# Optimization experiments

Measured on AMD Instinct MI355X. Metric: run time of the kernel, lower is better.

The kernel has to match this reference:

```python
import jax, jax.numpy as jnp
import numpy as np

N = 20000      # nodes
E = 256000     # edges
ESM = 1280     # esm_dim
H = 4          # heads
C = 256        # hidden_dim (per-head out)
HC = H * C     # 1024, concat width


def setup_inputs() -> dict:
    key = jax.random.key(0)
    ks = jax.random.split(key, 12)
    s = 0.02
    x = jax.random.normal(ks[0], (N, ESM), jnp.float32)
    edge_index = jax.random.randint(ks[1], (2, E), 0, N, dtype=jnp.int32)
    edge_weights = jax.random.uniform(ks[2], (E,), jnp.float32)
    # GATv2Conv params (PyG): lin_l (src, bias), lin_r (dst, no bias), lin_edge (no bias), att, out bias
    Wl = jax.random.normal(ks[3], (ESM, HC), jnp.float32) * s
    bl = jnp.zeros((HC,), jnp.float32)
    Wr = jax.random.normal(ks[4], (ESM, HC), jnp.float32) * s
    We = jax.random.normal(ks[5], (1, HC), jnp.float32) * s
    att = jax.random.normal(ks[6], (H, C), jnp.float32) * s
    b_gat = jnp.zeros((HC,), jnp.float32)
    # SAGEConv params: lin_l on mean-aggregated neighbors (bias), lin_r on root (no bias)
    Wsl = jax.random.normal(ks[7], (HC, ESM), jnp.float32) * s
    bsl = jnp.zeros((ESM,), jnp.float32)
    Wsr = jax.random.normal(ks[8], (HC, ESM), jnp.float32) * s
    # LayerNorm
    gamma = jnp.ones((ESM,), jnp.float32)
    beta = jnp.zeros((ESM,), jnp.float32)
    return dict(x=x, edge_index=edge_index, edge_weights=edge_weights,
                Wl=Wl, bl=bl, Wr=Wr, We=We, att=att, b_gat=b_gat,
                Wsl=Wsl, bsl=bsl, Wsr=Wsr, gamma=gamma, beta=beta)


def reference(x, edge_index, edge_weights, Wl, bl, Wr, We, att, b_gat,
              Wsl, bsl, Wsr, gamma, beta):
    src, dst = edge_index[0], edge_index[1]
    ew = edge_weights[:, None]                                    # [E,1]
    ones = jnp.ones((E,), x.dtype)
    deg = jax.ops.segment_sum(ones, dst, num_segments=N)          # in-degree [N]
    # ---- GATv2: add self-loops, edge_attr fill_value='mean' (mean of incoming attrs)
    loop_attr = jax.ops.segment_sum(ew, dst, num_segments=N) / jnp.maximum(deg, 1.0)[:, None]
    loop = jnp.arange(N, dtype=src.dtype)
    src_f = jnp.concatenate([src, loop])
    dst_f = jnp.concatenate([dst, loop])
    ea = jnp.concatenate([ew, loop_attr], axis=0)                 # [E+N,1]
    xl = (x @ Wl + bl).reshape(N, H, C)                           # source transform
    xr = (x @ Wr).reshape(N, H, C)                                # target transform
    ee = (ea @ We).reshape(-1, H, C)                              # edge transform
    m = jax.nn.leaky_relu(xl[src_f] + xr[dst_f] + ee, 0.2)        # [E+N,H,C]
    logits = jnp.einsum('ehc,hc->eh', m, att)                     # [E+N,H]
    amax = jax.ops.segment_max(logits, dst_f, num_segments=N)
    ex = jnp.exp(logits - amax[dst_f])
    den = jax.ops.segment_sum(ex, dst_f, num_segments=N)
    alpha = ex / (den[dst_f] + 1e-16)                             # softmax per dst node
    gat = jax.ops.segment_sum(alpha[:, :, None] * xl[src_f], dst_f, num_segments=N)
    gat = gat.reshape(N, HC) + b_gat
    h = jax.nn.elu(gat)
    # ---- SAGEConv: mean neighbor aggregation (no self loops) + root weight
    agg = jax.ops.segment_sum(h[src], dst, num_segments=N) / jnp.maximum(deg, 1.0)[:, None]
    y = jax.nn.relu(agg @ Wsl + bsl + h @ Wsr)
    # ---- residual + LayerNorm
    z = y + x
    mu = jnp.mean(z, axis=-1, keepdims=True)
    var = jnp.mean(jnp.square(z - mu), axis=-1, keepdims=True)
    return (z - mu) * jax.lax.rsqrt(var + 1e-5) * gamma + beta
```

## Files before the change

kernel.cpp:

```cpp
#include <hip/hip_runtime.h>
#include <hip/hip_bf16.h>
#include <math.h>

constexpr int kN   = 20000;
constexpr int kE   = 256000;
constexpr int kESM = 1280;
constexpr int kHC  = 1024;

typedef unsigned int  u32;
typedef unsigned short ushort_t;
typedef __bf16 bf16x8 __attribute__((ext_vector_type(8)));
typedef float  f32x4  __attribute__((ext_vector_type(4)));
typedef unsigned short u16x8 __attribute__((ext_vector_type(8)));
typedef unsigned short u16x4 __attribute__((ext_vector_type(4)));
typedef __attribute__((address_space(1))) const u32 gu32;
typedef __attribute__((address_space(3))) u32 lu32;

static __device__ __forceinline__ unsigned short f2bf_rne(float f) {
    u32 u = __float_as_uint(f);
    u32 r = (u + 0x7FFFu + ((u >> 16) & 1u)) >> 16;
    return (unsigned short)r;
}
static __device__ __forceinline__ float bf2f(unsigned short h) {
    return __uint_as_float(((u32)h) << 16);
}

__global__ __launch_bounds__(256) void deg_kernel(
    const int* __restrict__ dst, const float* __restrict__ ew,
    int* __restrict__ deg, float* __restrict__ wsum)
{
    int e = blockIdx.x * 256 + threadIdx.x;
    if (e < kE) {
        int d = dst[e];
        atomicAdd(&deg[d], 1);
        atomicAdd(&wsum[d], ew[e]);
    }
}

__global__ __launch_bounds__(256) void scan_kernel(
    const int* __restrict__ deg, float* __restrict__ loopat,
    int* __restrict__ offsets)
{
    __shared__ int s[256];
    int tid = threadIdx.x;
    int base = 0;
    if (tid == 0) offsets[0] = 0;
    for (int t0 = 0; t0 < kN; t0 += 256) {
        int i = t0 + tid;
        int d = (i < kN) ? deg[i] : 0;
        if (i < kN) {
            float w = loopat[i];
            loopat[i] = w / fmaxf((float)d, 1.0f);
        }
        s[tid] = d;
        int v = d;
        for (int off = 1; off < 256; off <<= 1) {
            __syncthreads();
            int add = (tid >= off) ? s[tid - off] : 0;
            __syncthreads();
            v += add;
            s[tid] = v;
        }
        __syncthreads();
        if (i < kN) offsets[i + 1] = base + v;
        base += s[255];
        __syncthreads();
    }
}

__global__ __launch_bounds__(256) void sort_kernel(
    const int* __restrict__ src, const int* __restrict__ dst,
    const float* __restrict__ ew, const int* __restrict__ offsets,
    int* __restrict__ cnt, int* __restrict__ ssrc, float* __restrict__ sew)
{
    int e = blockIdx.x * 256 + threadIdx.x;
    if (e < kE) {
        int d = dst[e];
        int p = offsets[d] + atomicAdd(&cnt[d], 1);
        ssrc[p] = src[e];
        sew[p]  = ew[e];
    }
}


__global__ __launch_bounds__(512) void pack_a_kernel(
    const float* __restrict__ A, int M, int K,
    int NKB, ushort_t* __restrict__ dst)
{
    const int kb = blockIdx.x, mb = blockIdx.y;
    const int tid = threadIdx.x;
    const int g = tid >> 7, r = tid & 127;
    const int row = mb * 128 + r;

    u16x8 hi, lo;
    if (row < M) {
        const float* src = A + (size_t)row * K + kb * 32 + g * 8;
        float4 v0 = *(const float4*)src;
        float4 v1 = *(const float4*)(src + 4);
        float vals[8] = {v0.x, v0.y, v0.z, v0.w, v1.x, v1.y, v1.z, v1.w};
#pragma unroll
        for (int j = 0; j < 8; ++j) {
            unsigned short h = f2bf_rne(vals[j]);
            hi[j] = h;
            lo[j] = f2bf_rne(vals[j] - bf2f(h));
        }
    } else {
#pragma unroll
        for (int j = 0; j < 8; ++j) { hi[j] = 0; lo[j] = 0; }
    }
    ushort_t* tb = dst + ((size_t)mb * NKB + kb) * 8192;
    *(u16x8*)&tb[0    + g * 1024 + r * 8] = hi;
    *(u16x8*)&tb[4096 + g * 1024 + r * 8] = lo;
}

__global__ __launch_bounds__(512) void pack_a2_kernel(
    const float* __restrict__ agg, const ushort_t* __restrict__ hb,
    int M, ushort_t* __restrict__ dst)
{
    const int kb = blockIdx.x, mb = blockIdx.y;
    const int tid = threadIdx.x;
    const int g = tid >> 7, r = tid & 127;
    const int row = mb * 128 + r;

    u16x8 hi, lo;
    if (row < M) {
        if (kb < 32) {
            const float* src = agg + (size_t)row * 1024 + kb * 32 + g * 8;
            float4 v0 = *(const float4*)src;
            float4 v1 = *(const float4*)(src + 4);
            float vals[8] = {v0.x, v0.y, v0.z, v0.w, v1.x, v1.y, v1.z, v1.w};
#pragma unroll
            for (int j = 0; j < 8; ++j) {
                unsigned short h = f2bf_rne(vals[j]);
                hi[j] = h;
                lo[j] = f2bf_rne(vals[j] - bf2f(h));
            }
        } else {
            hi = *(const u16x8*)&hb[(size_t)row * 1024 + (kb - 32) * 32 + g * 8];
#pragma unroll
            for (int j = 0; j < 8; ++j) lo[j] = 0;
        }
    } else {
#pragma unroll
        for (int j = 0; j < 8; ++j) { hi[j] = 0; lo[j] = 0; }
    }
    ushort_t* tb = dst + ((size_t)mb * 64 + kb) * 8192;
    *(u16x8*)&tb[0    + g * 1024 + r * 8] = hi;
    *(u16x8*)&tb[4096 + g * 1024 + r * 8] = lo;
}

__global__ __launch_bounds__(512) void pack_b_kernel(
    const float* __restrict__ B1, const float* __restrict__ B2,
    int N, int split, int mode, ushort_t* __restrict__ dst)
{
    const int kb = blockIdx.x, nb = blockIdx.y;
    const int NKB = gridDim.x;
    const int tid = threadIdx.x;
    const int g = tid >> 7, c = tid & 127;
    const int n = nb * 128 + c;

    u16x8 hi, lo;
#pragma unroll
    for (int j = 0; j < 8; ++j) {
        int k = kb * 32 + g * 8 + j;
        float v;
        if (mode == 0) {
            v = (n < split) ? B1[(size_t)k * split + n]
                            : B2[(size_t)k * (N - split) + (n - split)];
        } else {
            v = (k < split) ? B1[(size_t)k * N + n]
                            : B2[(size_t)(k - split) * N + n];
        }
        unsigned short h = f2bf_rne(v);
        hi[j] = h;
        lo[j] = f2bf_rne(v - bf2f(h));
    }
    ushort_t* tb = dst + ((size_t)nb * NKB + kb) * 8192;
    *(u16x8*)&tb[0    + g * 1024 + c * 8] = hi;
    *(u16x8*)&tb[4096 + g * 1024 + c * 8] = lo;
}

__global__ __launch_bounds__(256) void gemm_mfma(
    const ushort_t* __restrict__ Ap, const ushort_t* __restrict__ Bp,
    const float* __restrict__ bias, int biasN,
    const float* __restrict__ resid, float* __restrict__ C,
    int M, int N, int NKB, int do_relu)
{
    __shared__ ushort_t sb[16384];
    const int tid  = threadIdx.x;
    const int wid  = tid >> 6;
    const int lane = tid & 63;
    const int l15 = lane & 15, l4 = lane >> 4;
    const int mb = blockIdx.y, nb = blockIdx.x;
    const int wr = wid >> 1, wc = wid & 1;

    f32x4 acc[4][4];
#pragma unroll
    for (int i = 0; i < 4; ++i)
#pragma unroll
        for (int j = 0; j < 4; ++j) acc[i][j] = (f32x4){0.f, 0.f, 0.f, 0.f};

    const char* at = (const char*)(Ap + (size_t)mb * NKB * 8192);
    const char* bt = (const char*)(Bp + (size_t)nb * NKB * 8192);

    for (int kb = 0; kb < NKB; ++kb) {
        const char* atk = at + (size_t)kb * 16384;
        const char* btk = bt + (size_t)kb * 16384;
#pragma unroll
        for (int c = 0; c < 4; ++c) {
            __builtin_amdgcn_global_load_lds(
                (gu32*)(atk + c * 4096 + tid * 16),
                (lu32*)&sb[c * 2048 + wid * 512], 16, 0, 0);
            __builtin_amdgcn_global_load_lds(
                (gu32*)(btk + c * 4096 + tid * 16),
                (lu32*)&sb[8192 + c * 2048 + wid * 512], 16, 0, 0);
        }
        __syncthreads();

        bf16x8 af[2][4], bv[2][4];
#pragma unroll
        for (int hl = 0; hl < 2; ++hl)
#pragma unroll
            for (int m = 0; m < 4; ++m)
                af[hl][m] = *(const bf16x8*)&sb[hl * 4096 + l4 * 1024 + (wr * 64 + m * 16 + l15) * 8];
#pragma unroll
        for (int hl = 0; hl < 2; ++hl)
#pragma unroll
            for (int n = 0; n < 4; ++n)
                bv[hl][n] = *(const bf16x8*)&sb[8192 + hl * 4096 + l4 * 1024 + (wc * 64 + n * 16 + l15) * 8];

#pragma unroll
        for (int m = 0; m < 4; ++m)
#pragma unroll
            for (int n = 0; n < 4; ++n) {
                acc[m][n] = __builtin_amdgcn_mfma_f32_16x16x32_bf16(af[0][m], bv[0][n], acc[m][n], 0, 0, 0);
                acc[m][n] = __builtin_amdgcn_mfma_f32_16x16x32_bf16(af[0][m], bv[1][n], acc[m][n], 0, 0, 0);
                acc[m][n] = __builtin_amdgcn_mfma_f32_16x16x32_bf16(af[1][m], bv[0][n], acc[m][n], 0, 0, 0);
            }
        __syncthreads();
    }

    const int row_w = mb * 128 + wr * 64;
    const int col_w = nb * 128 + wc * 64;
#pragma unroll
    for (int m = 0; m < 4; ++m) {
#pragma unroll
        for (int n = 0; n < 4; ++n) {
            const int col = col_w + n * 16 + l15;
#pragma unroll
            for (int j = 0; j < 4; ++j) {
                const int row = row_w + m * 16 + l4 * 4 + j;
                if (row < M) {
                    float v = acc[m][n][j];
                    if (bias && col < biasN) v += bias[col];
                    if (do_relu) v = fmaxf(v, 0.f);
                    if (resid) v += resid[(size_t)row * N + col];
                    C[(size_t)row * N + col] = v;
                }
            }
        }
    }
}

__global__ __launch_bounds__(256) void gat2_kernel(
    const float* __restrict__ xlr, const int* __restrict__ ssrc,
    const float* __restrict__ sew, const int* __restrict__ offsets,
    const float* __restrict__ loopat, const float* __restrict__ We,
    const float* __restrict__ att, const float* __restrict__ bgat,
    ushort_t* __restrict__ hout)
{
    const int n = blockIdx.x;
    const int base = threadIdx.x * 4;

    const float4 xr4 = *(const float4*)&xlr[(size_t)n * 2048 + 1024 + base];
    const float4 We4 = *(const float4*)&We[base];
    const float4 at4 = *(const float4*)&att[base];

    float M = -INFINITY, D = 0.f;
    float4 acc = make_float4(0.f, 0.f, 0.f, 0.f);

    const int beg = offsets[n], end = offsets[n + 1];
    for (int e = beg; e <= end; ++e) {
        int s; float w;
        if (e < end) { s = ssrc[e]; w = sew[e]; }
        else         { s = n;       w = loopat[n]; }

        const float4 xls = *(const float4*)&xlr[(size_t)s * 2048 + base];
        float m0 = xls.x + xr4.x + w * We4.x;
        float m1 = xls.y + xr4.y + w * We4.y;
        float m2 = xls.z + xr4.z + w * We4.z;
        float m3 = xls.w + xr4.w + w * We4.w;
        m0 = (m0 >= 0.f) ? m0 : 0.2f * m0;
        m1 = (m1 >= 0.f) ? m1 : 0.2f * m1;
        m2 = (m2 >= 0.f) ? m2 : 0.2f * m2;
        m3 = (m3 >= 0.f) ? m3 : 0.2f * m3;
        float p = m0 * at4.x + m1 * at4.y + m2 * at4.z + m3 * at4.w;
#pragma unroll
        for (int o = 32; o >= 1; o >>= 1) p += __shfl_xor(p, o, 64);

        float newM  = fmaxf(M, p);
        float scale = __expf(M - newM);
        float wexp  = __expf(p - newM);
        D     = D * scale + wexp;
        acc.x = acc.x * scale + wexp * xls.x;
        acc.y = acc.y * scale + wexp * xls.y;
        acc.z = acc.z * scale + wexp * xls.z;
        acc.w = acc.w * scale + wexp * xls.w;
        M = newM;
    }

    const float inv = 1.0f / (D + 1e-16f);
    float g0 = acc.x * inv + bgat[base + 0];
    float g1 = acc.y * inv + bgat[base + 1];
    float g2 = acc.z * inv + bgat[base + 2];
    float g3 = acc.w * inv + bgat[base + 3];
    u16x4 hv;
    hv[0] = f2bf_rne((g0 > 0.f) ? g0 : expm1f(g0));
    hv[1] = f2bf_rne((g1 > 0.f) ? g1 : expm1f(g1));
    hv[2] = f2bf_rne((g2 > 0.f) ? g2 : expm1f(g2));
    hv[3] = f2bf_rne((g3 > 0.f) ? g3 : expm1f(g3));
    *(u16x4*)&hout[(size_t)n * 1024 + base] = hv;
}

__global__ __launch_bounds__(256) void agg2_kernel(
    const ushort_t* __restrict__ hb, const int* __restrict__ ssrc,
    const int* __restrict__ offsets, float* __restrict__ aggout)
{
    const int n = blockIdx.x;
    const int base = threadIdx.x * 4;
    float4 a = make_float4(0.f, 0.f, 0.f, 0.f);
    const int beg = offsets[n], end = offsets[n + 1];
    for (int e = beg; e < end; ++e) {
        const u16x4 hv = *(const u16x4*)&hb[(size_t)ssrc[e] * 1024 + base];
        a.x += bf2f(hv[0]); a.y += bf2f(hv[1]);
        a.z += bf2f(hv[2]); a.w += bf2f(hv[3]);
    }
    const float inv = 1.0f / fmaxf((float)(end - beg), 1.0f);
    a.x *= inv; a.y *= inv; a.z *= inv; a.w *= inv;
    *(float4*)&aggout[(size_t)n * 1024 + base] = a;
}

__global__ __launch_bounds__(320) void ln_kernel(
    float* __restrict__ z, const float* __restrict__ gamma,
    const float* __restrict__ beta)
{
    const int r = blockIdx.x;
    const int t = threadIdx.x;
    const int wave = t >> 6, lane = t & 63;
    __shared__ float red[5];

    float4 v = *(const float4*)&z[(size_t)r * kESM + t * 4];
    float s = v.x + v.y + v.z + v.w;
#pragma unroll
    for (int o = 32; o >= 1; o >>= 1) s += __shfl_xor(s, o, 64);
    if (lane == 0) red[wave] = s;
    __syncthreads();
    s = red[0] + red[1] + red[2] + red[3] + red[4];
    const float mu = s * (1.0f / (float)kESM);

    float dx = v.x - mu, dy = v.y - mu, dz = v.z - mu, dw = v.w - mu;
    float q = dx * dx + dy * dy + dz * dz + dw * dw;
#pragma unroll
    for (int o = 32; o >= 1; o >>= 1) q += __shfl_xor(q, o, 64);
    __syncthreads();
    if (lane == 0) red[wave] = q;
    __syncthreads();
    q = red[0] + red[1] + red[2] + red[3] + red[4];
    const float rstd = rsqrtf(q * (1.0f / (float)kESM) + 1e-5f);

    const float4 g4 = *(const float4*)&gamma[t * 4];
    const float4 b4 = *(const float4*)&beta[t * 4];
    float4 o;
    o.x = dx * rstd * g4.x + b4.x;
    o.y = dy * rstd * g4.y + b4.y;
    o.z = dz * rstd * g4.z + b4.z;
    o.w = dw * rstd * g4.w + b4.w;
    *(float4*)&z[(size_t)r * kESM + t * 4] = o;
}

#define BM 128
#define BN 128
#define BK 16

__global__ __launch_bounds__(256) void gemm_kernel(
    const float* __restrict__ A,  const float* __restrict__ B,
    const float* __restrict__ A2, const float* __restrict__ B2,
    const float* __restrict__ bias, const float* __restrict__ resid,
    float* __restrict__ C, int M, int N, int K, int do_relu)
{
    __shared__ float As[BK][BM];
    __shared__ float Bs[BK][BN];

    const int tid = threadIdx.x;
    const int bm = blockIdx.y, bn = blockIdx.x;
    const int row0 = bm * BM, col0 = bn * BN;
    const int tx = tid & 15, ty = tid >> 4;

    float acc[8][8];
#pragma unroll
    for (int i = 0; i < 8; ++i)
#pragma unroll
        for (int j = 0; j < 8; ++j) acc[i][j] = 0.0f;

    const int arow  = tid >> 1;
    const int akoff = (tid & 1) * 8;
    const int bkr   = tid >> 4;
    const int bcol  = (tid & 15) * 8;

    for (int pair = 0; pair < 2; ++pair) {
        const float* Ap = pair ? A2 : A;
        const float* Bp = pair ? B2 : B;
        if (!Ap) break;
        for (int k0 = 0; k0 < K; k0 += BK) {
            float4 a0 = make_float4(0.f, 0.f, 0.f, 0.f);
            float4 a1 = a0;
            int gr = row0 + arow;
            if (gr < M) {
                const float* aptr = Ap + (size_t)gr * K + k0 + akoff;
                a0 = *(const float4*)aptr;
                a1 = *(const float4*)(aptr + 4);
            }
            const float* bptr = Bp + (size_t)(k0 + bkr) * N + col0 + bcol;
            float4 b0 = *(const float4*)bptr;
            float4 b1 = *(const float4*)(bptr + 4);

            __syncthreads();
            As[akoff + 0][arow] = a0.x;
            As[akoff + 1][arow] = a0.y;
            As[akoff + 2][arow] = a0.z;
            As[akoff + 3][arow] = a0.w;
            As[akoff + 4][arow] = a1.x;
            As[akoff + 5][arow] = a1.y;
            As[akoff + 6][arow] = a1.z;
            As[akoff + 7][arow] = a1.w;
            *(float4*)&Bs[bkr][bcol]     = b0;
            *(float4*)&Bs[bkr][bcol + 4] = b1;
            __syncthreads();

#pragma unroll
            for (int kk = 0; kk < BK; ++kk) {
                float4 a0r = *(const float4*)&As[kk][ty * 8];
                float4 a1r = *(const float4*)&As[kk][ty * 8 + 4];
                float4 b0r = *(const float4*)&Bs[kk][tx * 4];
                float4 b1r = *(const float4*)&Bs[kk][64 + tx * 4];
                float ar[8] = {a0r.x, a0r.y, a0r.z, a0r.w, a1r.x, a1r.y, a1r.z, a1r.w};
                float br[8] = {b0r.x, b0r.y, b0r.z, b0r.w, b1r.x, b1r.y, b1r.z, b1r.w};
#pragma unroll
                for (int i = 0; i < 8; ++i)
#pragma unroll
                    for (int j = 0; j < 8; ++j)
                        acc[i][j] = fmaf(ar[i], br[j], acc[i][j]);
            }
        }
    }

#pragma unroll
    for (int i = 0; i < 8; ++i) {
        int gr = row0 + ty * 8 + i;
        if (gr >= M) break;
#pragma unroll
        for (int half = 0; half < 2; ++half) {
            int gc = col0 + half * 64 + tx * 4;
            float4 out;
            float* o = &out.x;
            const float* rrow = resid ? (resid + (size_t)gr * N + gc) : nullptr;
#pragma unroll
            for (int j = 0; j < 4; ++j) {
                float v = acc[i][half * 4 + j];
                if (bias) v += bias[gc + j];
                if (do_relu) v = fmaxf(v, 0.0f);
                if (rrow) v += rrow[j];
                o[j] = v;
            }
            *(float4*)&C[(size_t)gr * N + gc] = out;
        }
    }
}

__global__ __launch_bounds__(256) void gat_kernel(
    const float* __restrict__ xl, const float* __restrict__ xr,
    const int* __restrict__ ssrc, const float* __restrict__ sew,
    const int* __restrict__ offsets, const float* __restrict__ loopat,
    const float* __restrict__ We, const float* __restrict__ att,
    const float* __restrict__ bgat, float* __restrict__ hout)
{
    const int n = blockIdx.x;
    const int base = threadIdx.x * 4;

    const float4 xr4 = *(const float4*)&xr[(size_t)n * kHC + base];
    const float4 We4 = *(const float4*)&We[base];
    const float4 at4 = *(const float4*)&att[base];

    float M = -INFINITY, D = 0.f;
    float4 acc = make_float4(0.f, 0.f, 0.f, 0.f);

    const int beg = offsets[n], end = offsets[n + 1];
    for (int e = beg; e <= end; ++e) {
        int s; float w;
        if (e < end) { s = ssrc[e]; w = sew[e]; }
        else         { s = n;       w = loopat[n]; }

        const float4 xls = *(const float4*)&xl[(size_t)s * kHC + base];
        float m0 = xls.x + xr4.x + w * We4.x;
        float m1 = xls.y + xr4.y + w * We4.y;
        float m2 = xls.z + xr4.z + w * We4.z;
        float m3 = xls.w + xr4.w + w * We4.w;
        m0 = (m0 >= 0.f) ? m0 : 0.2f * m0;
        m1 = (m1 >= 0.f) ? m1 : 0.2f * m1;
        m2 = (m2 >= 0.f) ? m2 : 0.2f * m2;
        m3 = (m3 >= 0.f) ? m3 : 0.2f * m3;
        float p = m0 * at4.x + m1 * at4.y + m2 * at4.z + m3 * at4.w;
#pragma unroll
        for (int o = 32; o >= 1; o >>= 1) p += __shfl_xor(p, o, 64);

        float newM  = fmaxf(M, p);
        float scale = __expf(M - newM);
        float wexp  = __expf(p - newM);
        D     = D * scale + wexp;
        acc.x = acc.x * scale + wexp * xls.x;
        acc.y = acc.y * scale + wexp * xls.y;
        acc.z = acc.z * scale + wexp * xls.z;
        acc.w = acc.w * scale + wexp * xls.w;
        M = newM;
    }

    const float inv = 1.0f / (D + 1e-16f);
    float g0 = acc.x * inv + bgat[base + 0];
    float g1 = acc.y * inv + bgat[base + 1];
    float g2 = acc.z * inv + bgat[base + 2];
    float g3 = acc.w * inv + bgat[base + 3];
    float4 hv;
    hv.x = (g0 > 0.f) ? g0 : expm1f(g0);
    hv.y = (g1 > 0.f) ? g1 : expm1f(g1);
    hv.z = (g2 > 0.f) ? g2 : expm1f(g2);
    hv.w = (g3 > 0.f) ? g3 : expm1f(g3);
    *(float4*)&hout[(size_t)n * kHC + base] = hv;
}

__global__ __launch_bounds__(256) void agg_kernel(
    const float* __restrict__ h, const int* __restrict__ ssrc,
    const int* __restrict__ offsets, float* __restrict__ aggout)
{
    const int n = blockIdx.x;
    const int base = threadIdx.x * 4;
    float4 a = make_float4(0.f, 0.f, 0.f, 0.f);
    const int beg = offsets[n], end = offsets[n + 1];
    for (int e = beg; e < end; ++e) {
        const float4 hv = *(const float4*)&h[(size_t)ssrc[e] * kHC + base];
        a.x += hv.x; a.y += hv.y; a.z += hv.z; a.w += hv.w;
    }
    const float inv = 1.0f / fmaxf((float)(end - beg), 1.0f);
    a.x *= inv; a.y *= inv; a.z *= inv; a.w *= inv;
    *(float4*)&aggout[(size_t)n * kHC + base] = a;
}

extern "C" void kernel_launch(void* const* d_in, const int* in_sizes, int n_in,
                              void* d_out, int out_size, void* d_ws, size_t ws_size,
                              hipStream_t stream)
{
    const float* x     = (const float*)d_in[0];
    const int*   ei    = (const int*)  d_in[1];
    const float* ew    = (const float*)d_in[2];
    const float* Wl    = (const float*)d_in[3];
    const float* bl    = (const float*)d_in[4];
    const float* Wr    = (const float*)d_in[5];
    const float* We    = (const float*)d_in[6];
    const float* att   = (const float*)d_in[7];
    const float* bgat  = (const float*)d_in[8];
    const float* Wsl   = (const float*)d_in[9];
    const float* bsl   = (const float*)d_in[10];
    const float* Wsr   = (const float*)d_in[11];
    const float* gamma = (const float*)d_in[12];
    const float* beta  = (const float*)d_in[13];
    const int* src = ei;
    const int* dst = ei + kE;
    char* ws = (char*)d_ws;

    const size_t SZ_XPACK = (size_t)157 * 40 * 16384;
    const size_t SZ_XLR   = (size_t)kN * 2048 * 4;
    const size_t SZ_HBUF  = (size_t)kN * 1024 * 2;
    const size_t SZ_B1    = (size_t)16 * 40 * 16384;
    const size_t SZ_B2    = (size_t)10 * 64 * 16384;
    const size_t OFF_XLR  = SZ_XPACK;
    const size_t OFF_HBUF = OFF_XLR + SZ_XLR;
    const size_t OFF_B1   = OFF_HBUF + SZ_HBUF;
    const size_t OFF_B2   = OFF_B1 + SZ_B1;
    size_t off = OFF_B2 + SZ_B2;
    auto salloc = [&](size_t bytes) -> void* {
        void* p = ws + off;
        off = (off + bytes + 255) & ~(size_t)255;
        return p;
    };
    int*   deg    = (int*)  salloc((size_t)kN * 4);
    int*   cnt    = (int*)  salloc((size_t)kN * 4);
    int*   offs   = (int*)  salloc((size_t)(kN + 1) * 4);
    float* loopat = (float*)salloc((size_t)kN * 4);
    int*   ssrc   = (int*)  salloc((size_t)kE * 4);
    float* sew    = (float*)salloc((size_t)kE * 4);
    const size_t FAST_TOTAL = off;

    if (ws_size >= FAST_TOTAL) {
        ushort_t* xpack = (ushort_t*)(ws);
        float*    xlr   = (float*)   (ws + OFF_XLR);
        ushort_t* hbuf  = (ushort_t*)(ws + OFF_HBUF);
        ushort_t* b1p   = (ushort_t*)(ws + OFF_B1);
        ushort_t* b2p   = (ushort_t*)(ws + OFF_B2);
        float*    aggb  = (float*)   (ws + OFF_HBUF - (size_t)kN * 1024 * 4);
        ushort_t* apack = (ushort_t*)(ws);

        hipMemsetAsync(deg,    0, (size_t)kN * 4, stream);
        hipMemsetAsync(cnt,    0, (size_t)kN * 4, stream);
        hipMemsetAsync(loopat, 0, (size_t)kN * 4, stream);

        deg_kernel <<<(kE + 255) / 256, 256, 0, stream>>>(dst, ew, deg, loopat);
        scan_kernel<<<1, 256, 0, stream>>>(deg, loopat, offs);
        sort_kernel<<<(kE + 255) / 256, 256, 0, stream>>>(src, dst, ew, offs, cnt, ssrc, sew);

        pack_a_kernel<<<dim3(40, 157), 512, 0, stream>>>(x, kN, kESM, 40, xpack);
        pack_b_kernel<<<dim3(40, 16), 512, 0, stream>>>(Wl, Wr, 2048, 1024, 0, b1p);
        pack_b_kernel<<<dim3(64, 10), 512, 0, stream>>>(Wsl, Wsr, 1280, 1024, 1, b2p);

        gemm_mfma<<<dim3(16, 157), 256, 0, stream>>>(xpack, b1p, bl, 1024,
                                                     nullptr, xlr, kN, 2048, 40, 0);

        gat2_kernel<<<kN, 256, 0, stream>>>(xlr, ssrc, sew, offs, loopat,
                                            We, att, bgat, hbuf);
        agg2_kernel<<<kN, 256, 0, stream>>>(hbuf, ssrc, offs, aggb);

        pack_a2_kernel<<<dim3(64, 157), 512, 0, stream>>>(aggb, hbuf, kN, apack);

        gemm_mfma<<<dim3(10, 157), 256, 0, stream>>>(apack, b2p, bsl, 1280,
                                                     x, (float*)d_out, kN, 1280, 64, 1);

        ln_kernel<<<kN, 320, 0, stream>>>((float*)d_out, gamma, beta);
    } else {
        size_t foff = 0;
        auto falloc = [&](size_t bytes) -> void* {
            void* p = ws + foff;
            foff = (foff + bytes + 255) & ~(size_t)255;
            return p;
        };
        int*   fdeg    = (int*)  falloc((size_t)kN * 4);
        int*   fcnt    = (int*)  falloc((size_t)kN * 4);
        int*   foffs   = (int*)  falloc((size_t)(kN + 1) * 4);
        float* floopat = (float*)falloc((size_t)kN * 4);
        int*   fssrc   = (int*)  falloc((size_t)kE * 4);
        float* fsew    = (float*)falloc((size_t)kE * 4);
        float* bufA    = (float*)falloc((size_t)kN * kHC * 4);
        float* bufB    = (float*)falloc((size_t)kN * kHC * 4);

        hipMemsetAsync(fdeg,    0, (size_t)kN * 4, stream);
        hipMemsetAsync(fcnt,    0, (size_t)kN * 4, stream);
        hipMemsetAsync(floopat, 0, (size_t)kN * 4, stream);

        deg_kernel <<<(kE + 255) / 256, 256, 0, stream>>>(dst, ew, fdeg, floopat);
        scan_kernel<<<1, 256, 0, stream>>>(fdeg, floopat, foffs);
        sort_kernel<<<(kE + 255) / 256, 256, 0, stream>>>(src, dst, ew, foffs, fcnt, fssrc, fsew);

        dim3 g1(kHC / BN, (kN + BM - 1) / BM);
        gemm_kernel<<<g1, 256, 0, stream>>>(x, Wl, nullptr, nullptr, bl, nullptr,
                                            bufA, kN, kHC, kESM, 0);
        gemm_kernel<<<g1, 256, 0, stream>>>(x, Wr, nullptr, nullptr, nullptr, nullptr,
                                            bufB, kN, kHC, kESM, 0);

        gat_kernel<<<kN, 256, 0, stream>>>(bufA, bufB, fssrc, fsew, foffs, floopat,
                                           We, att, bgat, bufB);
        agg_kernel<<<kN, 256, 0, stream>>>(bufB, fssrc, foffs, bufA);

        dim3 g2(kESM / BN, (kN + BM - 1) / BM);
        gemm_kernel<<<g2, 256, 0, stream>>>(bufA, Wsl, bufB, Wsr, bsl, x,
                                            (float*)d_out, kN, kESM, kHC, 1);

        ln_kernel<<<kN, 320, 0, stream>>>((float*)d_out, gamma, beta);
    }
}
```

Before: 1.460 ms.

## Skip zero lo-half of h operand in SAGE GEMM and swizzle blocks across XCDs

The second GEMM's A operand has an all-zero low bf16 half for the h (root) columns, so a dedicated K-loop for those blocks now loads only the hi A half and issues two MFMAs instead of three. The pack kernel no longer writes the zero lo half for those blocks. Workgroup IDs are also remapped so consecutive tiles land on the same XCD, aiming for better L2 reuse. This cuts MFMA work and global traffic for half of the K range at the cost of a second loop body and more code.

```diff
diff --git a/kernel.cpp b/kernel.cpp
--- a/kernel.cpp
+++ b/kernel.cpp
@@ -121,10 +121,11 @@
     const int tid = threadIdx.x;
     const int g = tid >> 7, r = tid & 127;
     const int row = mb * 128 + r;
-
-    u16x8 hi, lo;
-    if (row < M) {
-        if (kb < 32) {
+    ushort_t* tb = dst + ((size_t)mb * 64 + kb) * 8192;
+
+    if (kb < 32) {
+        u16x8 hi, lo;
+        if (row < M) {
             const float* src = agg + (size_t)row * 1024 + kb * 32 + g * 8;
             float4 v0 = *(const float4*)src;
             float4 v1 = *(const float4*)(src + 4);
@@ -136,17 +137,21 @@
                 lo[j] = f2bf_rne(vals[j] - bf2f(h));
             }
         } else {
+#pragma unroll
+            for (int j = 0; j < 8; ++j) { hi[j] = 0; lo[j] = 0; }
+        }
+        *(u16x8*)&tb[0    + g * 1024 + r * 8] = hi;
+        *(u16x8*)&tb[4096 + g * 1024 + r * 8] = lo;
+    } else {
+        u16x8 hi;
+        if (row < M) {
             hi = *(const u16x8*)&hb[(size_t)row * 1024 + (kb - 32) * 32 + g * 8];
-#pragma unroll
-            for (int j = 0; j < 8; ++j) lo[j] = 0;
-        }
-    } else {
-#pragma unroll
-        for (int j = 0; j < 8; ++j) { hi[j] = 0; lo[j] = 0; }
-    }
-    ushort_t* tb = dst + ((size_t)mb * 64 + kb) * 8192;
-    *(u16x8*)&tb[0    + g * 1024 + r * 8] = hi;
-    *(u16x8*)&tb[4096 + g * 1024 + r * 8] = lo;
+        } else {
+#pragma unroll
+            for (int j = 0; j < 8; ++j) hi[j] = 0;
+        }
+        *(u16x8*)&tb[0 + g * 1024 + r * 8] = hi;
+    }
 }
 
 __global__ __launch_bounds__(512) void pack_b_kernel(
@@ -184,14 +189,20 @@
     const ushort_t* __restrict__ Ap, const ushort_t* __restrict__ Bp,
     const float* __restrict__ bias, int biasN,
     const float* __restrict__ resid, float* __restrict__ C,
-    int M, int N, int NKB, int do_relu)
+    int M, int N, int NKB, int nkb_full, int do_relu)
 {
     __shared__ ushort_t sb[16384];
     const int tid  = threadIdx.x;
     const int wid  = tid >> 6;
     const int lane = tid & 63;
     const int l15 = lane & 15, l4 = lane >> 4;
-    const int mb = blockIdx.y, nb = blockIdx.x;
+
+    const int nwg = gridDim.x * gridDim.y;
+    const int lin = blockIdx.y * gridDim.x + blockIdx.x;
+    const int q = nwg >> 3, r = nwg & 7;
+    const int xcd = lin & 7, pos = lin >> 3;
+    const int swz = (xcd < r ? xcd * (q + 1) : r * (q + 1) + (xcd - r) * q) + pos;
+    const int mb = swz / gridDim.x, nb = swz % gridDim.x;
     const int wr = wid >> 1, wc = wid & 1;
 
     f32x4 acc[4][4];
@@ -203,7 +214,7 @@
     const char* at = (const char*)(Ap + (size_t)mb * NKB * 8192);
     const char* bt = (const char*)(Bp + (size_t)nb * NKB * 8192);
 
-    for (int kb = 0; kb < NKB; ++kb) {
+    for (int kb = 0; kb < nkb_full; ++kb) {
         const char* atk = at + (size_t)kb * 16384;
         const char* btk = bt + (size_t)kb * 16384;
 #pragma unroll
@@ -236,6 +247,43 @@
                 acc[m][n] = __builtin_amdgcn_mfma_f32_16x16x32_bf16(af[0][m], bv[0][n], acc[m][n], 0, 0, 0);
                 acc[m][n] = __builtin_amdgcn_mfma_f32_16x16x32_bf16(af[0][m], bv[1][n], acc[m][n], 0, 0, 0);
                 acc[m][n] = __builtin_amdgcn_mfma_f32_16x16x32_bf16(af[1][m], bv[0][n], acc[m][n], 0, 0, 0);
+            }
+        __syncthreads();
+    }
+
+    for (int kb = nkb_full; kb < NKB; ++kb) {
+        const char* atk = at + (size_t)kb * 16384;
+        const char* btk = bt + (size_t)kb * 16384;
+#pragma unroll
+        for (int c = 0; c < 2; ++c) {
+            __builtin_amdgcn_global_load_lds(
+                (gu32*)(atk + c * 4096 + tid * 16),
+                (lu32*)&sb[c * 2048 + wid * 512], 16, 0, 0);
+        }
+#pragma unroll
+        for (int c = 0; c < 4; ++c) {
+            __builtin_amdgcn_global_load_lds(
+                (gu32*)(btk + c * 4096 + tid * 16),
+                (lu32*)&sb[8192 + c * 2048 + wid * 512], 16, 0, 0);
+        }
+        __syncthreads();
+
+        bf16x8 af0[4], bv[2][4];
+#pragma unroll
+        for (int m = 0; m < 4; ++m)
+            af0[m] = *(const bf16x8*)&sb[l4 * 1024 + (wr * 64 + m * 16 + l15) * 8];
+#pragma unroll
+        for (int hl = 0; hl < 2; ++hl)
+#pragma unroll
+            for (int n = 0; n < 4; ++n)
+                bv[hl][n] = *(const bf16x8*)&sb[8192 + hl * 4096 + l4 * 1024 + (wc * 64 + n * 16 + l15) * 8];
+
+#pragma unroll
+        for (int m = 0; m < 4; ++m)
+#pragma unroll
+            for (int n = 0; n < 4; ++n) {
+                acc[m][n] = __builtin_amdgcn_mfma_f32_16x16x32_bf16(af0[m], bv[0][n], acc[m][n], 0, 0, 0);
+                acc[m][n] = __builtin_amdgcn_mfma_f32_16x16x32_bf16(af0[m], bv[1][n], acc[m][n], 0, 0, 0);
             }
         __syncthreads();
     }
@@ -621,7 +669,7 @@
         pack_b_kernel<<<dim3(64, 10), 512, 0, stream>>>(Wsl, Wsr, 1280, 1024, 1, b2p);
 
         gemm_mfma<<<dim3(16, 157), 256, 0, stream>>>(xpack, b1p, bl, 1024,
-                                                     nullptr, xlr, kN, 2048, 40, 0);
+                                                     nullptr, xlr, kN, 2048, 40, 40, 0);
 
         gat2_kernel<<<kN, 256, 0, stream>>>(xlr, ssrc, sew, offs, loopat,
                                             We, att, bgat, hbuf);
@@ -630,7 +678,7 @@
         pack_a2_kernel<<<dim3(64, 157), 512, 0, stream>>>(aggb, hbuf, kN, apack);
 
         gemm_mfma<<<dim3(10, 157), 256, 0, stream>>>(apack, b2p, bsl, 1280,
-                                                     x, (float*)d_out, kN, 1280, 64, 1);
+                                                     x, (float*)d_out, kN, 1280, 64, 32, 1);
 
         ln_kernel<<<kN, 320, 0, stream>>>((float*)d_out, gamma, beta);
     } else {
```

New measurement: 1.405 ms. 1.04x faster.
